# Optimization experiments

Measured on AMD Instinct MI355X. Metric: run time of the kernel, lower is better.

Reference implementation:

```python
import jax, jax.numpy as jnp
import numpy as np

N_NODES = 100000
N_EDGES = 1000000
N_GRAPHS = 512
HID = 64
EDIM = 32
LAYERS = 4
BN_EPS = 1e-5


def _batchnorm(x, g, b):
    # training-mode BatchNorm1d: biased batch statistics over the node axis
    m = x.mean(axis=0)
    v = jnp.var(x, axis=0)
    return (x - m) * jax.lax.rsqrt(v + BN_EPS) * g + b


def setup_inputs() -> dict:
    key = jax.random.key(0)
    ks = jax.random.split(key, 16)
    zw = 2 * HID + EDIM  # 160: cat([x_i, x_j, e_ij])
    inp = {
        "z": jax.random.randint(ks[0], (N_NODES,), 0, 100),
        "edge_index": jax.random.randint(ks[1], (2, N_EDGES), 0, N_NODES),
        "edge_attr": jax.random.normal(ks[2], (N_EDGES, EDIM), dtype=jnp.float32),
        "batch_ids": jnp.sort(jax.random.randint(ks[3], (N_NODES,), 0, N_GRAPHS)),
        "emb": jax.random.normal(ks[4], (100, HID), dtype=jnp.float32),
        "Wf": jax.random.normal(ks[5], (LAYERS, zw, HID), dtype=jnp.float32) / np.sqrt(zw),
        "bf": jnp.zeros((LAYERS, HID), jnp.float32),
        "Ws": jax.random.normal(ks[6], (LAYERS, zw, HID), dtype=jnp.float32) / np.sqrt(zw),
        "bs": jnp.zeros((LAYERS, HID), jnp.float32),
        "g_cbn": jnp.ones((LAYERS, HID), jnp.float32),
        "b_cbn": jnp.zeros((LAYERS, HID), jnp.float32),
        "g_obn": jnp.ones((LAYERS, HID), jnp.float32),
        "b_obn": jnp.zeros((LAYERS, HID), jnp.float32),
        "W1": jax.random.normal(ks[7], (HID, HID), dtype=jnp.float32) / np.sqrt(HID),
        "b1": jnp.zeros((HID,), jnp.float32),
        "W2": jax.random.normal(ks[8], (HID, 1), dtype=jnp.float32) / np.sqrt(HID),
        "b2": jnp.zeros((1,), jnp.float32),
    }
    return inp


def reference(z, edge_index, edge_attr, batch_ids, emb, Wf, bf, Ws, bs,
              g_cbn, b_cbn, g_obn, b_obn, W1, b1, W2, b2):
    src = edge_index[0]  # x_j (source)
    dst = edge_index[1]  # x_i (target / aggregation index)
    x = emb[z]  # [N, HID]
    for l in range(LAYERS):
        # CGConv message: z_e = cat([x_i, x_j, e_ij]); m = sigmoid(f(z_e)) * softplus(s(z_e))
        z_e = jnp.concatenate([x[dst], x[src], edge_attr], axis=-1)  # [E, 160]
        msg = jax.nn.sigmoid(z_e @ Wf[l] + bf[l]) * jax.nn.softplus(z_e @ Ws[l] + bs[l])
        agg = jax.ops.segment_sum(msg, dst, num_segments=N_NODES)  # [N, HID]
        agg = _batchnorm(agg, g_cbn[l], b_cbn[l])  # CGConv's internal BN
        x = agg + x  # residual
        x = _batchnorm(x, g_obn[l], b_obn[l])  # outer BatchNorm1d
        x = jax.nn.softplus(x)
    # global mean pool over graphs
    sums = jax.ops.segment_sum(x, batch_ids, num_segments=N_GRAPHS)
    cnts = jax.ops.segment_sum(jnp.ones((N_NODES,), x.dtype), batch_ids, num_segments=N_GRAPHS)
    pooled = sums / jnp.maximum(cnts, 1.0)[:, None]
    h = jax.nn.silu(pooled @ W1 + b1)  # dropout is identity in eval mode
    out = (h @ W2 + b2)[:, 0]
    return out
```

## Files before the change

kernel.cpp:

```cpp
#include <hip/hip_runtime.h>
#include <cstdint>
#include <cstddef>

#define N_NODES 100000
#define N_EDGES 1000000
#define N_GRAPHS 512
#define HID 64
#define EDIM 32
#define LAYERS 4
#define BN_EPS 1e-5

static const size_t X_OFF    = 0;
static const size_t AGG_OFF  = X_OFF + 25600000;
static const size_t STA_OFF  = AGG_OFF + 25600000;
static const size_t STB_OFF  = STA_OFF + 1024;
static const size_t POOL_OFF = STB_OFF + 1024;
static const size_t CNT_OFF  = POOL_OFF + 131072;
static const size_t DEG_OFF  = CNT_OFF + 2048;
static const size_t ECUR_OFF = DEG_OFF + 400128;
static const size_t PERM_OFF = ECUR_OFF + 400128;
static const size_t DSTS_OFF = PERM_OFF + 4000000;
static const size_t P_OFF    = DSTS_OFF + 4000000;

__device__ __forceinline__ float rl_f(float v, int k) {
    return __uint_as_float(__builtin_amdgcn_readlane(__float_as_uint(v), k));
}
__device__ __forceinline__ float sigmoidf_(float x) {
    return 1.f / (1.f + __expf(-x));
}
__device__ __forceinline__ float softplusf_(float x) {
    return fmaxf(x, 0.f) + __logf(1.f + __expf(-fabsf(x)));
}
__device__ __forceinline__ void fma4(float4& a, const float4& wv, float xv) {
    a.x = fmaf(xv, wv.x, a.x);
    a.y = fmaf(xv, wv.y, a.y);
    a.z = fmaf(xv, wv.z, a.z);
    a.w = fmaf(xv, wv.w, a.w);
}

__global__ __launch_bounds__(256) void cg_embed(const int* __restrict__ z,
                                                const float* __restrict__ emb,
                                                float* __restrict__ x) {
    int i = blockIdx.x * 256 + threadIdx.x;
    if (i < N_NODES * HID) {
        x[i] = emb[z[i >> 6] * HID + (i & 63)];
    }
}

__global__ __launch_bounds__(256) void cg_hist(const int* __restrict__ ei,
                                               int* __restrict__ deg) {
    int e = blockIdx.x * 256 + threadIdx.x;
    if (e < N_EDGES) atomicAdd(&deg[ei[N_EDGES + e]], 1);
}

#define SPAN 98
__global__ __launch_bounds__(1024) void cg_scan(const int* __restrict__ deg,
                                                int* __restrict__ ecur) {
    __shared__ int ps[1024];
    const int t = threadIdx.x;
    const int s0 = t * SPAN;
    int sum = 0;
    for (int i = 0; i < SPAN; i++) {
        int idx = s0 + i;
        if (idx < N_NODES) sum += deg[idx];
    }
    ps[t] = sum;
    __syncthreads();
    for (int off = 1; off < 1024; off <<= 1) {
        int v = (t >= off) ? ps[t - off] : 0;
        __syncthreads();
        ps[t] += v;
        __syncthreads();
    }
    int run = ps[t] - sum;
    for (int i = 0; i < SPAN; i++) {
        int idx = s0 + i;
        if (idx < N_NODES) {
            ecur[idx] = run;
            run += deg[idx];
        }
    }
}

__global__ __launch_bounds__(256) void cg_scatter(const int* __restrict__ ei,
                                                  int* __restrict__ ecur,
                                                  int* __restrict__ perm,
                                                  int* __restrict__ dst_s) {
    int e = blockIdx.x * 256 + threadIdx.x;
    if (e < N_EDGES) {
        int d = ei[N_EDGES + e];
        int pos = atomicAdd(&ecur[d], 1);
        perm[pos] = e;
        dst_s[pos] = d;
    }
}

__global__ __launch_bounds__(256) void cg_nodeP4(const float* __restrict__ x,
                                                 const float* __restrict__ Wf,
                                                 const float* __restrict__ Ws,
                                                 float* __restrict__ P) {
    __shared__ __align__(16) float xs[64][68];
    const int tid = threadIdx.x;
    const int base = blockIdx.x * 64;
#pragma unroll
    for (int i = 0; i < 4; i++) {
        int f4 = tid * 4 + i;
        int r = f4 >> 4, c4 = (f4 & 15) * 4;
        float4 v = {0, 0, 0, 0};
        if (base + r < N_NODES) v = *(const float4*)(x + (size_t)(base + r) * HID + c4);
        *(float4*)(&xs[r][c4]) = v;
    }
    __syncthreads();

    const int c = tid & 15, g = tid >> 4;
    const int j4 = c * 4;
    float4 acc[4][4];
#pragma unroll
    for (int m = 0; m < 4; m++)
#pragma unroll
        for (int q = 0; q < 4; q++) acc[m][q] = {0, 0, 0, 0};

    for (int k = 0; k < 64; k++) {
        float4 w0 = *(const float4*)(Wf + (size_t)k * HID + j4);
        float4 w1 = *(const float4*)(Ws + (size_t)k * HID + j4);
        float4 w2 = *(const float4*)(Wf + (size_t)(64 + k) * HID + j4);
        float4 w3 = *(const float4*)(Ws + (size_t)(64 + k) * HID + j4);
#pragma unroll
        for (int m = 0; m < 4; m++) {
            float xv = xs[g + m * 16][k];
            fma4(acc[m][0], w0, xv);
            fma4(acc[m][1], w1, xv);
            fma4(acc[m][2], w2, xv);
            fma4(acc[m][3], w3, xv);
        }
    }
#pragma unroll
    for (int m = 0; m < 4; m++) {
        int r = base + g + m * 16;
        if (r < N_NODES) {
            float* o = P + (size_t)r * 256;
            *(float4*)(o + j4)       = acc[m][0];
            *(float4*)(o + 64 + j4)  = acc[m][1];
            *(float4*)(o + 128 + j4) = acc[m][2];
            *(float4*)(o + 192 + j4) = acc[m][3];
        }
    }
}

__global__ __launch_bounds__(256) void cg_edge2(const float* __restrict__ P,
                                                const int* __restrict__ ei,
                                                const float* __restrict__ ea,
                                                const int* __restrict__ perm,
                                                const int* __restrict__ dst_s,
                                                const float* __restrict__ WfE,
                                                const float* __restrict__ WsE,
                                                const float* __restrict__ bf,
                                                const float* __restrict__ bs,
                                                float* __restrict__ agg) {
    const int j = threadIdx.x & 63;
    float wfe[EDIM], wse[EDIM];
#pragma unroll
    for (int k = 0; k < EDIM; k++) {
        wfe[k] = WfE[k * HID + j];
        wse[k] = WsE[k * HID + j];
    }
    const float bfv = bf[j], bsv = bs[j];
    const int wave = blockIdx.x * 4 + (threadIdx.x >> 6);
    const int nw = gridDim.x * 4;
    const int chunk = (N_EDGES + nw - 1) / nw;
    const int e0 = wave * chunk;
    const int e1 = min(e0 + chunk, N_EDGES);
    if (e0 >= e1) return;

    int eu = __builtin_amdgcn_readfirstlane(e0);
    int d_c  = dst_s[eu];
    int pe_c = perm[eu];
    int s_c  = ei[pe_c];
    float er_c = ea[(size_t)pe_c * EDIM + (j & 31)];

    int cur = d_c;
    float pf0 = P[(size_t)cur * 256 + j];
    float ps0 = P[(size_t)cur * 256 + 64 + j];
    float acc = 0.f;

    for (int e = e0; e < e1; ++e) {
        const int d = d_c, srcn = s_c;
        const float er = er_c;
        if (e + 1 < e1) {
            int nu = __builtin_amdgcn_readfirstlane(e + 1);
            d_c  = dst_s[nu];
            pe_c = perm[nu];
            s_c  = ei[pe_c];
            er_c = ea[(size_t)pe_c * EDIM + (j & 31)];
        }
        if (d != cur) {
            unsafeAtomicAdd(&agg[(size_t)cur * HID + j], acc);
            acc = 0.f;
            cur = d;
            pf0 = P[(size_t)cur * 256 + j];
            ps0 = P[(size_t)cur * 256 + 64 + j];
        }
        const float sf = P[(size_t)srcn * 256 + 128 + j];
        const float ss = P[(size_t)srcn * 256 + 192 + j];
        float uf = bfv, us = bsv;
#pragma unroll
        for (int k = 0; k < EDIM; k++) {
            const float ek = rl_f(er, k);
            uf = fmaf(ek, wfe[k], uf);
            us = fmaf(ek, wse[k], us);
        }
        uf += pf0 + sf;
        us += ps0 + ss;
        acc += sigmoidf_(uf) * softplusf_(us);
    }
    unsafeAtomicAdd(&agg[(size_t)cur * HID + j], acc);
}

__global__ __launch_bounds__(256) void cg_stats(const float* __restrict__ a,
                                                double* __restrict__ st) {
    const int j = threadIdx.x & 63, rl = threadIdx.x >> 6;
    float s = 0.f, q = 0.f;
    for (int n = blockIdx.x * 4 + rl; n < N_NODES; n += gridDim.x * 4) {
        float v = a[(size_t)n * HID + j];
        s += v;
        q += v * v;
    }
    __shared__ float ls[4][64], lq[4][64];
    ls[rl][j] = s;
    lq[rl][j] = q;
    __syncthreads();
    if (threadIdx.x < 64) {
        float S = ls[0][j] + ls[1][j] + ls[2][j] + ls[3][j];
        float Q = lq[0][j] + lq[1][j] + lq[2][j] + lq[3][j];
        unsafeAtomicAdd(&st[j], (double)S);
        unsafeAtomicAdd(&st[64 + j], (double)Q);
    }
}

__global__ __launch_bounds__(256) void cg_bn1res(float* __restrict__ agg,
                                                 const float* __restrict__ x,
                                                 const float* __restrict__ g,
                                                 const float* __restrict__ b,
                                                 const double* __restrict__ stA,
                                                 double* __restrict__ stB) {
    const int j = threadIdx.x & 63, rl = threadIdx.x >> 6;
    const double mean = stA[j] * (1.0 / N_NODES);
    const double var  = stA[64 + j] * (1.0 / N_NODES) - mean * mean;
    const float sc = (float)((double)g[j] / sqrt(var + BN_EPS));
    const float sh = (float)((double)b[j] - mean * (double)sc);
    float s = 0.f, q = 0.f;
    for (int n = blockIdx.x * 4 + rl; n < N_NODES; n += gridDim.x * 4) {
        size_t idx = (size_t)n * HID + j;
        float v = fmaf(agg[idx], sc, sh) + x[idx];
        agg[idx] = v;
        s += v;
        q += v * v;
    }
    __shared__ float ls[4][64], lq[4][64];
    ls[rl][j] = s;
    lq[rl][j] = q;
    __syncthreads();
    if (threadIdx.x < 64) {
        float S = ls[0][j] + ls[1][j] + ls[2][j] + ls[3][j];
        float Q = lq[0][j] + lq[1][j] + lq[2][j] + lq[3][j];
        unsafeAtomicAdd(&stB[j], (double)S);
        unsafeAtomicAdd(&stB[64 + j], (double)Q);
    }
}

__global__ __launch_bounds__(256) void cg_bn2act(const float* __restrict__ agg,
                                                 float* __restrict__ x,
                                                 const float* __restrict__ g,
                                                 const float* __restrict__ b,
                                                 const double* __restrict__ stB) {
    const int j = threadIdx.x & 63, rl = threadIdx.x >> 6;
    const double mean = stB[j] * (1.0 / N_NODES);
    const double var  = stB[64 + j] * (1.0 / N_NODES) - mean * mean;
    const float sc = (float)((double)g[j] / sqrt(var + BN_EPS));
    const float sh = (float)((double)b[j] - mean * (double)sc);
    for (int n = blockIdx.x * 4 + rl; n < N_NODES; n += gridDim.x * 4) {
        size_t idx = (size_t)n * HID + j;
        x[idx] = softplusf_(fmaf(agg[idx], sc, sh));
    }
}

__global__ __launch_bounds__(256) void cg_pool(const float* __restrict__ x,
                                               const int* __restrict__ bid,
                                               float* __restrict__ pooled,
                                               float* __restrict__ cnt) {
    const int j = threadIdx.x & 63, rl = threadIdx.x >> 6;
    const int chunk = (N_NODES + gridDim.x - 1) / gridDim.x;
    const int s0 = blockIdx.x * chunk;
    const int e0 = min(s0 + chunk, N_NODES);
    float acc = 0.f, c = 0.f;
    int cur = -1;
    for (int n = s0 + rl; n < e0; n += 4) {
        int bg = bid[n];
        if (bg != cur) {
            if (cur >= 0) {
                unsafeAtomicAdd(&pooled[(size_t)cur * HID + j], acc);
                if (j == 0) unsafeAtomicAdd(&cnt[cur], c);
            }
            cur = bg;
            acc = 0.f;
            c = 0.f;
        }
        acc += x[(size_t)n * HID + j];
        c += 1.f;
    }
    if (cur >= 0) {
        unsafeAtomicAdd(&pooled[(size_t)cur * HID + j], acc);
        if (j == 0) unsafeAtomicAdd(&cnt[cur], c);
    }
}

__global__ __launch_bounds__(64) void cg_mlp(const float* __restrict__ pooled,
                                             const float* __restrict__ cnt,
                                             const float* __restrict__ W1,
                                             const float* __restrict__ b1,
                                             const float* __restrict__ W2,
                                             const float* __restrict__ b2,
                                             float* __restrict__ out) {
    const int g = blockIdx.x;
    const int j = threadIdx.x;
    const float c = fmaxf(cnt[g], 1.f);
    const float p = pooled[(size_t)g * HID + j] / c;
    float h = b1[j];
    for (int k = 0; k < HID; k++) {
        h = fmaf(rl_f(p, k), W1[k * HID + j], h);
    }
    const float hs = h * sigmoidf_(h);
    float v = hs * W2[j];
#pragma unroll
    for (int off = 32; off > 0; off >>= 1) v += __shfl_down(v, off);
    if (j == 0) out[g] = v + b2[0];
}

extern "C" void kernel_launch(void* const* d_in, const int* in_sizes, int n_in,
                              void* d_out, int out_size, void* d_ws, size_t ws_size,
                              hipStream_t stream) {
    const int*   z   = (const int*)d_in[0];
    const int*   ei  = (const int*)d_in[1];
    const float* ea  = (const float*)d_in[2];
    const int*   bid = (const int*)d_in[3];
    const float* emb = (const float*)d_in[4];
    const float* Wf  = (const float*)d_in[5];
    const float* bf  = (const float*)d_in[6];
    const float* Ws  = (const float*)d_in[7];
    const float* bs  = (const float*)d_in[8];
    const float* gc  = (const float*)d_in[9];
    const float* bc  = (const float*)d_in[10];
    const float* go  = (const float*)d_in[11];
    const float* bo  = (const float*)d_in[12];
    const float* W1  = (const float*)d_in[13];
    const float* b1  = (const float*)d_in[14];
    const float* W2  = (const float*)d_in[15];
    const float* b2  = (const float*)d_in[16];
    float* out = (float*)d_out;

    char* ws = (char*)d_ws;
    float*  x      = (float*)(ws + X_OFF);
    float*  agg    = (float*)(ws + AGG_OFF);
    double* stA    = (double*)(ws + STA_OFF);
    double* stB    = (double*)(ws + STB_OFF);
    float*  pooled = (float*)(ws + POOL_OFF);
    float*  cnt    = (float*)(ws + CNT_OFF);
    int*    deg    = (int*)(ws + DEG_OFF);
    int*    ecur   = (int*)(ws + ECUR_OFF);
    int*    perm   = (int*)(ws + PERM_OFF);
    int*    dst_s  = (int*)(ws + DSTS_OFF);
    float*  P      = (float*)(ws + P_OFF);

    (void)hipMemsetAsync(ws + DEG_OFF, 0, 400000, stream);
    cg_hist<<<(N_EDGES + 255) / 256, 256, 0, stream>>>(ei, deg);
    cg_scan<<<1, 1024, 0, stream>>>(deg, ecur);
    cg_scatter<<<(N_EDGES + 255) / 256, 256, 0, stream>>>(ei, ecur, perm, dst_s);

    cg_embed<<<(N_NODES * HID + 255) / 256, 256, 0, stream>>>(z, emb, x);

    for (int l = 0; l < LAYERS; l++) {
        const float* Wfl = Wf + (size_t)l * 160 * HID;
        const float* Wsl = Ws + (size_t)l * 160 * HID;
        (void)hipMemsetAsync(ws + AGG_OFF, 0, 25600000 + 2048, stream);
        cg_nodeP4<<<(N_NODES + 63) / 64, 256, 0, stream>>>(x, Wfl, Wsl, P);
        cg_edge2<<<4096, 256, 0, stream>>>(P, ei, ea, perm, dst_s,
                                           Wfl + 128 * HID, Wsl + 128 * HID,
                                           bf + l * HID, bs + l * HID, agg);
        cg_stats<<<1024, 256, 0, stream>>>(agg, stA);
        cg_bn1res<<<1024, 256, 0, stream>>>(agg, x, gc + l * HID, bc + l * HID, stA, stB);
        cg_bn2act<<<1024, 256, 0, stream>>>(agg, x, go + l * HID, bo + l * HID, stB);
    }

    (void)hipMemsetAsync(ws + POOL_OFF, 0, 131072 + 2048, stream);
    cg_pool<<<1024, 256, 0, stream>>>(x, bid, pooled, cnt);
    cg_mlp<<<N_GRAPHS, 64, 0, stream>>>(pooled, cnt, W1, b1, W2, b2, out);
}
```

Before: 2.493 ms.

## Parallelize degree scan, fold agg zeroing into BN kernel, simplify edge loop

Replaces the single-block serial prefix scan with a three-kernel block-sum/scan/apply scan. Removes the per-layer agg memset by zeroing agg inside cg_bn2act and resets the stats accumulators inside other kernels. The edge kernel drops its software prefetch, reads edge attributes directly from memory as uniform scalar loads instead of readlane broadcasts, halves the grid, and adds occupancy launch bounds. These target launch, memset and scan overhead, but the edge loop loses its latency hiding from the prefetch.

Result: faster. 2.398 ms (-3.8%).

```diff
diff --git a/kernel.cpp b/kernel.cpp
--- a/kernel.cpp
+++ b/kernel.cpp
@@ -20,7 +20,11 @@
 static const size_t ECUR_OFF = DEG_OFF + 400128;
 static const size_t PERM_OFF = ECUR_OFF + 400128;
 static const size_t DSTS_OFF = PERM_OFF + 4000000;
-static const size_t P_OFF    = DSTS_OFF + 4000000;
+static const size_t BSUM_OFF = DSTS_OFF + 4000000;
+static const size_t BOFF_OFF = BSUM_OFF + 2048;
+static const size_t P_OFF    = BOFF_OFF + 2048;
+
+#define SCAN_BLOCKS 391
 
 __device__ __forceinline__ float rl_f(float v, int k) {
     return __uint_as_float(__builtin_amdgcn_readlane(__float_as_uint(v), k));
@@ -53,33 +57,50 @@
     if (e < N_EDGES) atomicAdd(&deg[ei[N_EDGES + e]], 1);
 }
 
-#define SPAN 98
-__global__ __launch_bounds__(1024) void cg_scan(const int* __restrict__ deg,
+__global__ __launch_bounds__(256) void cg_bsum(const int* __restrict__ deg,
+                                               int* __restrict__ bsum) {
+    const int i = blockIdx.x * 256 + threadIdx.x;
+    int v = (i < N_NODES) ? deg[i] : 0;
+#pragma unroll
+    for (int off = 32; off > 0; off >>= 1) v += __shfl_down(v, off);
+    __shared__ int wsum[4];
+    if ((threadIdx.x & 63) == 0) wsum[threadIdx.x >> 6] = v;
+    __syncthreads();
+    if (threadIdx.x == 0) bsum[blockIdx.x] = wsum[0] + wsum[1] + wsum[2] + wsum[3];
+}
+
+__global__ __launch_bounds__(512) void cg_bscan(const int* __restrict__ bsum,
+                                                int* __restrict__ boff) {
+    __shared__ int ps[512];
+    const int t = threadIdx.x;
+    int v = (t < SCAN_BLOCKS) ? bsum[t] : 0;
+    ps[t] = v;
+    __syncthreads();
+    for (int off = 1; off < 512; off <<= 1) {
+        int u = (t >= off) ? ps[t - off] : 0;
+        __syncthreads();
+        ps[t] += u;
+        __syncthreads();
+    }
+    if (t < SCAN_BLOCKS) boff[t] = ps[t] - v;
+}
+
+__global__ __launch_bounds__(256) void cg_escan(const int* __restrict__ deg,
+                                                const int* __restrict__ boff,
                                                 int* __restrict__ ecur) {
-    __shared__ int ps[1024];
+    __shared__ int ps[256];
     const int t = threadIdx.x;
-    const int s0 = t * SPAN;
-    int sum = 0;
-    for (int i = 0; i < SPAN; i++) {
-        int idx = s0 + i;
-        if (idx < N_NODES) sum += deg[idx];
-    }
-    ps[t] = sum;
-    __syncthreads();
-    for (int off = 1; off < 1024; off <<= 1) {
-        int v = (t >= off) ? ps[t - off] : 0;
+    const int i = blockIdx.x * 256 + t;
+    int v = (i < N_NODES) ? deg[i] : 0;
+    ps[t] = v;
+    __syncthreads();
+    for (int off = 1; off < 256; off <<= 1) {
+        int u = (t >= off) ? ps[t - off] : 0;
         __syncthreads();
-        ps[t] += v;
+        ps[t] += u;
         __syncthreads();
     }
-    int run = ps[t] - sum;
-    for (int i = 0; i < SPAN; i++) {
-        int idx = s0 + i;
-        if (idx < N_NODES) {
-            ecur[idx] = run;
-            run += deg[idx];
-        }
-    }
+    if (i < N_NODES) ecur[i] = ps[t] - v + boff[blockIdx.x];
 }
 
 __global__ __launch_bounds__(256) void cg_scatter(const int* __restrict__ ei,
@@ -95,10 +116,10 @@
     }
 }
 
-__global__ __launch_bounds__(256) void cg_nodeP4(const float* __restrict__ x,
-                                                 const float* __restrict__ Wf,
-                                                 const float* __restrict__ Ws,
-                                                 float* __restrict__ P) {
+__global__ __launch_bounds__(256, 4) void cg_nodeP4(const float* __restrict__ x,
+                                                    const float* __restrict__ Wf,
+                                                    const float* __restrict__ Ws,
+                                                    float* __restrict__ P) {
     __shared__ __align__(16) float xs[64][68];
     const int tid = threadIdx.x;
     const int base = blockIdx.x * 64;
@@ -112,8 +133,8 @@
     }
     __syncthreads();
 
-    const int c = tid & 15, g = tid >> 4;
-    const int j4 = c * 4;
+    const int g = tid >> 4;
+    const int j4 = (tid & 15) * 4;
     float4 acc[4][4];
 #pragma unroll
     for (int m = 0; m < 4; m++)
@@ -147,16 +168,16 @@
     }
 }
 
-__global__ __launch_bounds__(256) void cg_edge2(const float* __restrict__ P,
-                                                const int* __restrict__ ei,
-                                                const float* __restrict__ ea,
-                                                const int* __restrict__ perm,
-                                                const int* __restrict__ dst_s,
-                                                const float* __restrict__ WfE,
-                                                const float* __restrict__ WsE,
-                                                const float* __restrict__ bf,
-                                                const float* __restrict__ bs,
-                                                float* __restrict__ agg) {
+__global__ __launch_bounds__(256, 4) void cg_edge3(const float* __restrict__ P,
+                                                   const int* __restrict__ ei,
+                                                   const float* __restrict__ ea,
+                                                   const int* __restrict__ perm,
+                                                   const int* __restrict__ dst_s,
+                                                   const float* __restrict__ WfE,
+                                                   const float* __restrict__ WsE,
+                                                   const float* __restrict__ bf,
+                                                   const float* __restrict__ bs,
+                                                   float* __restrict__ agg) {
     const int j = threadIdx.x & 63;
     float wfe[EDIM], wse[EDIM];
 #pragma unroll
@@ -172,27 +193,14 @@
     const int e1 = min(e0 + chunk, N_EDGES);
     if (e0 >= e1) return;
 
-    int eu = __builtin_amdgcn_readfirstlane(e0);
-    int d_c  = dst_s[eu];
-    int pe_c = perm[eu];
-    int s_c  = ei[pe_c];
-    float er_c = ea[(size_t)pe_c * EDIM + (j & 31)];
-
-    int cur = d_c;
+    int cur = __builtin_amdgcn_readfirstlane(dst_s[e0]);
     float pf0 = P[(size_t)cur * 256 + j];
     float ps0 = P[(size_t)cur * 256 + 64 + j];
     float acc = 0.f;
 
     for (int e = e0; e < e1; ++e) {
-        const int d = d_c, srcn = s_c;
-        const float er = er_c;
-        if (e + 1 < e1) {
-            int nu = __builtin_amdgcn_readfirstlane(e + 1);
-            d_c  = dst_s[nu];
-            pe_c = perm[nu];
-            s_c  = ei[pe_c];
-            er_c = ea[(size_t)pe_c * EDIM + (j & 31)];
-        }
+        const int d  = __builtin_amdgcn_readfirstlane(dst_s[e]);
+        const int pe = __builtin_amdgcn_readfirstlane(perm[e]);
         if (d != cur) {
             unsafeAtomicAdd(&agg[(size_t)cur * HID + j], acc);
             acc = 0.f;
@@ -200,24 +208,27 @@
             pf0 = P[(size_t)cur * 256 + j];
             ps0 = P[(size_t)cur * 256 + 64 + j];
         }
-        const float sf = P[(size_t)srcn * 256 + 128 + j];
-        const float ss = P[(size_t)srcn * 256 + 192 + j];
-        float uf = bfv, us = bsv;
+        const int s = __builtin_amdgcn_readfirstlane(ei[pe]);
+        const float sf = P[(size_t)s * 256 + 128 + j];
+        const float ss = P[(size_t)s * 256 + 192 + j];
+        const float* __restrict__ earow = ea + (size_t)pe * EDIM;
+        float uf = bfv + pf0 + sf;
+        float us = bsv + ps0 + ss;
 #pragma unroll
         for (int k = 0; k < EDIM; k++) {
-            const float ek = rl_f(er, k);
+            const float ek = earow[k];
             uf = fmaf(ek, wfe[k], uf);
             us = fmaf(ek, wse[k], us);
         }
-        uf += pf0 + sf;
-        us += ps0 + ss;
         acc += sigmoidf_(uf) * softplusf_(us);
     }
     unsafeAtomicAdd(&agg[(size_t)cur * HID + j], acc);
 }
 
 __global__ __launch_bounds__(256) void cg_stats(const float* __restrict__ a,
-                                                double* __restrict__ st) {
+                                                double* __restrict__ stA,
+                                                double* __restrict__ stB) {
+    if (blockIdx.x == 0 && threadIdx.x < 128) stB[threadIdx.x] = 0.0;
     const int j = threadIdx.x & 63, rl = threadIdx.x >> 6;
     float s = 0.f, q = 0.f;
     for (int n = blockIdx.x * 4 + rl; n < N_NODES; n += gridDim.x * 4) {
@@ -232,8 +243,8 @@
     if (threadIdx.x < 64) {
         float S = ls[0][j] + ls[1][j] + ls[2][j] + ls[3][j];
         float Q = lq[0][j] + lq[1][j] + lq[2][j] + lq[3][j];
-        unsafeAtomicAdd(&st[j], (double)S);
-        unsafeAtomicAdd(&st[64 + j], (double)Q);
+        unsafeAtomicAdd(&stA[j], (double)S);
+        unsafeAtomicAdd(&stA[64 + j], (double)Q);
     }
 }
 
@@ -268,11 +279,13 @@
     }
 }
 
-__global__ __launch_bounds__(256) void cg_bn2act(const float* __restrict__ agg,
+__global__ __launch_bounds__(256) void cg_bn2act(float* __restrict__ agg,
                                                  float* __restrict__ x,
                                                  const float* __restrict__ g,
                                                  const float* __restrict__ b,
-                                                 const double* __restrict__ stB) {
+                                                 const double* __restrict__ stB,
+                                                 double* __restrict__ stA) {
+    if (blockIdx.x == 0 && threadIdx.x < 128) stA[threadIdx.x] = 0.0;
     const int j = threadIdx.x & 63, rl = threadIdx.x >> 6;
     const double mean = stB[j] * (1.0 / N_NODES);
     const double var  = stB[64 + j] * (1.0 / N_NODES) - mean * mean;
@@ -281,6 +294,7 @@
     for (int n = blockIdx.x * 4 + rl; n < N_NODES; n += gridDim.x * 4) {
         size_t idx = (size_t)n * HID + j;
         x[idx] = softplusf_(fmaf(agg[idx], sc, sh));
+        agg[idx] = 0.f;
     }
 }
 
@@ -369,11 +383,18 @@
     int*    ecur   = (int*)(ws + ECUR_OFF);
     int*    perm   = (int*)(ws + PERM_OFF);
     int*    dst_s  = (int*)(ws + DSTS_OFF);
+    int*    bsum   = (int*)(ws + BSUM_OFF);
+    int*    boff   = (int*)(ws + BOFF_OFF);
     float*  P      = (float*)(ws + P_OFF);
 
+    (void)hipMemsetAsync(ws + AGG_OFF, 0, 25600000 + 2048, stream);
+    (void)hipMemsetAsync(ws + POOL_OFF, 0, 131072 + 2048, stream);
     (void)hipMemsetAsync(ws + DEG_OFF, 0, 400000, stream);
+
     cg_hist<<<(N_EDGES + 255) / 256, 256, 0, stream>>>(ei, deg);
-    cg_scan<<<1, 1024, 0, stream>>>(deg, ecur);
+    cg_bsum<<<SCAN_BLOCKS, 256, 0, stream>>>(deg, bsum);
+    cg_bscan<<<1, 512, 0, stream>>>(bsum, boff);
+    cg_escan<<<SCAN_BLOCKS, 256, 0, stream>>>(deg, boff, ecur);
     cg_scatter<<<(N_EDGES + 255) / 256, 256, 0, stream>>>(ei, ecur, perm, dst_s);
 
     cg_embed<<<(N_NODES * HID + 255) / 256, 256, 0, stream>>>(z, emb, x);
@@ -381,17 +402,15 @@
     for (int l = 0; l < LAYERS; l++) {
         const float* Wfl = Wf + (size_t)l * 160 * HID;
         const float* Wsl = Ws + (size_t)l * 160 * HID;
-        (void)hipMemsetAsync(ws + AGG_OFF, 0, 25600000 + 2048, stream);
         cg_nodeP4<<<(N_NODES + 63) / 64, 256, 0, stream>>>(x, Wfl, Wsl, P);
-        cg_edge2<<<4096, 256, 0, stream>>>(P, ei, ea, perm, dst_s,
+        cg_edge3<<<2048, 256, 0, stream>>>(P, ei, ea, perm, dst_s,
                                            Wfl + 128 * HID, Wsl + 128 * HID,
                                            bf + l * HID, bs + l * HID, agg);
-        cg_stats<<<1024, 256, 0, stream>>>(agg, stA);
+        cg_stats<<<1024, 256, 0, stream>>>(agg, stA, stB);
         cg_bn1res<<<1024, 256, 0, stream>>>(agg, x, gc + l * HID, bc + l * HID, stA, stB);
-        cg_bn2act<<<1024, 256, 0, stream>>>(agg, x, go + l * HID, bo + l * HID, stB);
-    }
-
-    (void)hipMemsetAsync(ws + POOL_OFF, 0, 131072 + 2048, stream);
+        cg_bn2act<<<1024, 256, 0, stream>>>(agg, x, go + l * HID, bo + l * HID, stB, stA);
+    }
+
     cg_pool<<<1024, 256, 0, stream>>>(x, bid, pooled, cnt);
     cg_mlp<<<N_GRAPHS, 64, 0, stream>>>(pooled, cnt, W1, b1, W2, b2, out);
 }
```
